# Kernel optimization log

Hardware: AMD Instinct MI355X
Metric: run time of the kernel (lower is better)

The kernel has to match this reference:

```python
import jax, jax.numpy as jnp
import numpy as np
import math

B, H, W = 4, 224, 224
NFEAT = 2048
N_SP, N_FAM, N_ORD = 200, 38, 13
THRESH = 0.5


def _conv(x, w, b, s):
    y = jax.lax.conv_general_dilated(x, w, (s, s), 'SAME', dimension_numbers=('NCHW', 'OIHW', 'NCHW'))
    return y + b[None, :, None, None]


def _features(x, bw1, bb1, bw2, bb2, bw3, bb3, bw4, bb4):
    # stride-32 CNN backbone standing in for nn.Sequential(*model.children()[:-2]) (2048-ch output)
    x = jax.nn.relu(_conv(x, bw1, bb1, 4))
    x = jax.nn.relu(_conv(x, bw2, bb2, 2))
    x = jax.nn.relu(_conv(x, bw3, bb3, 2))
    x = jax.nn.relu(_conv(x, bw4, bb4, 2))
    return x


def _resize_ac(img, y1, y2, x1, x2, oh, ow):
    # bilinear, align_corners=True resample of img[:, y1:y2, x1:x2] -> (C, oh, ow); jit-safe (gather, no dynamic shapes)
    Hh, Ww = img.shape[1], img.shape[2]
    ys = y1 + jnp.arange(oh, dtype=jnp.float32) * (y2 - 1 - y1) / (oh - 1)
    xs = x1 + jnp.arange(ow, dtype=jnp.float32) * (x2 - 1 - x1) / (ow - 1)
    ylo = jnp.clip(jnp.floor(ys).astype(jnp.int32), 0, Hh - 1)
    yhi = jnp.clip(ylo + 1, 0, Hh - 1)
    yf = (ys - ylo)[None, :, None]
    rows = img[:, ylo, :] * (1 - yf) + img[:, yhi, :] * yf
    xlo = jnp.clip(jnp.floor(xs).astype(jnp.int32), 0, Ww - 1)
    xhi = jnp.clip(xlo + 1, 0, Ww - 1)
    xf = (xs - xlo)[None, None, :]
    return rows[:, :, xlo] * (1 - xf) + rows[:, :, xhi] * xf


def _obj_loc(score, threshold):
    # vectorized, sync-free version of the torch obj_loc interval search
    n = score.shape[0]
    minsize = int(math.ceil(n * 0.125))
    defmax = int(math.ceil(n * 0.875))
    snorm = jnp.sign(score - threshold)
    cross = jnp.abs(snorm[1:] - snorm[:-1]) == 2  # crossing between j and j+1 -> index j+1 starts... torch puts index j in next interval
    ind = jnp.concatenate([cross, jnp.zeros((1,), bool)]).astype(jnp.int32)
    seg = jnp.cumsum(ind)  # segment id per position; matches torch half-open intervals [p_i, p_{i+1})
    k = jnp.sum(ind)       # number of crossings
    idx = jnp.arange(n, dtype=jnp.int32)
    seg_max = jax.ops.segment_max(score, seg, num_segments=n)
    seg_len = jax.ops.segment_sum(jnp.ones((n,), jnp.int32), seg, num_segments=n)
    seg_start = jax.ops.segment_min(idx, seg, num_segments=n)
    seg_end = jax.ops.segment_max(idx, seg, num_segments=n) + 1
    valid = (idx <= k) & (seg_len > 0)
    # torch processing order: first interval, then last, then interiors; ties keep earlier-processed
    order = jnp.where(idx == 0, 0, jnp.where(idx == k, 1, idx + 1))
    m = jnp.where(valid, seg_max, -jnp.inf)
    c1 = valid & (m == jnp.max(m))
    best_len = jnp.max(jnp.where(c1, seg_len, -1))
    c2 = c1 & (seg_len == best_len)
    sel = jnp.argmin(jnp.where(c2, order, n + 2))
    zmin, zmax = seg_start[sel], seg_end[sel]
    # min-size padding, exactly mirroring the sequential torch ifs
    pad = minsize - (zmax - zmin)
    hp = (pad + 1) // 2  # ceil(pad/2)
    need = (zmax - zmin) <= minsize
    cA = need & (zmin > hp) & (n - zmax > pad)
    zmin = jnp.where(cA, zmin - hp + 1, zmin)
    zmax = jnp.where(cA, zmax + hp, zmax)
    cB = need & (zmin < hp)
    zmin = jnp.where(cB, 0, zmin)
    zmax = jnp.where(cB, minsize, zmax)
    cC = need & (n - zmax < hp)
    zmin = jnp.where(cC, n - minsize + 1, zmin)
    zmax = jnp.where(cC, n, zmax)
    # no crossings -> fixed central window (torch early return)
    zmin = jnp.where(k == 0, minsize, zmin)
    zmax = jnp.where(k == 0, defmax, zmax)
    return zmin, zmax


def _norm01(v):
    mn, mx = v.min(), v.max()
    den = jnp.where(mx == mn, mx, mx - mn)
    num = jnp.where(mx == mn, v, v - mn)
    return num / den


def _w_h(gs, wscore, hscore, inputs, threshold):
    def one(g, wsc, hsc, img):
        top = jnp.argmax(g)  # == sort(descending)[0]
        x1, x2 = _obj_loc(_norm01(wsc[top]), threshold)
        y1, y2 = _obj_loc(_norm01(hsc[top]), threshold)
        return _resize_ac(img, y1, y2, x1, x2, img.shape[1], img.shape[2])
    return jax.vmap(one)(gs, wscore, hscore, inputs)


def _stage(gvec, fmap, inputs, wc, bc, wc1, bc1, lf_prev, bb):
    gf = gvec @ wc.T + bc  # conv1x1 on pooled feature == linear
    cam = jax.nn.sigmoid(jnp.einsum('bchw,oc->bohw', jax.lax.stop_gradient(fmap), wc) + bc[None, :, None, None])
    fh, fw = fmap.shape[2], fmap.shape[3]
    cam_up = jax.vmap(lambda im: _resize_ac(im, 0, fh, 0, fw, H, W))(cam)  # (B,C,H,W)
    wsc = cam_up.max(axis=2)  # max_pool2d((h,1)) -> (B,C,W)
    hsc = cam_up.max(axis=3)  # max_pool2d((1,w)) -> (B,C,H)
    lin = _w_h(gf, wsc, hsc, inputs, THRESH)
    la = _features(jax.lax.stop_gradient(lin), *bb)
    lf = la.mean(axis=(2, 3))  # AdaptiveAvgPool2d(1)
    ls = lf @ wc1.T + bc1
    if lf_prev is not None:
        ls = ls + (lf_prev @ wc1.T + bc1)  # bias added twice, as in torch
    return (gf + ls) / 2.0, lf


def _forward(inputs, bw1, bb1, bw2, bb2, bw3, bb3, bw4, bb4, w_ord, b_ord, w_ord1, b_ord1, w_fam, b_fam, w_fam1, b_fam1, w_sp, b_sp, w_sp1, b_sp1):
    bb = (bw1, bb1, bw2, bb2, bw3, bb3, bw4, bb4)
    fmap = _features(inputs, *bb)
    gvec = fmap.mean(axis=(2, 3))
    f_ord, lf_ord = _stage(gvec, fmap, inputs, w_ord, b_ord, w_ord1, b_ord1, None, bb)
    f_fam, lf_fam = _stage(gvec, fmap, inputs, w_fam, b_fam, w_fam1, b_fam1, lf_ord, bb)
    f_sp, _ = _stage(gvec, fmap, inputs, w_sp, b_sp, w_sp1, b_sp1, lf_fam, bb)
    return f_sp, f_fam, f_ord


def setup_inputs() -> dict:
    ks = jax.random.split(jax.random.key(0), 16)
    def he(k, shape, fan_in):
        return jax.random.normal(k, shape, jnp.float32) * np.float32(np.sqrt(2.0 / fan_in))
    d = {"inputs": jax.random.normal(ks[0], (B, 3, H, W), jnp.float32)}
    d["bw1"], d["bb1"] = he(ks[1], (256, 3, 7, 7), 3 * 49), jnp.zeros((256,), jnp.float32)
    d["bw2"], d["bb2"] = he(ks[2], (512, 256, 3, 3), 256 * 9), jnp.zeros((512,), jnp.float32)
    d["bw3"], d["bb3"] = he(ks[3], (1024, 512, 1, 1), 512), jnp.zeros((1024,), jnp.float32)
    d["bw4"], d["bb4"] = he(ks[4], (2048, 1024, 1, 1), 1024), jnp.zeros((2048,), jnp.float32)
    for i, (nm, nc) in enumerate([("ord", N_ORD), ("fam", N_FAM), ("sp", N_SP)]):
        d["w_" + nm] = he(ks[5 + 2 * i], (nc, NFEAT), NFEAT)
        d["b_" + nm] = jnp.zeros((nc,), jnp.float32)
        d["w_" + nm + "1"] = he(ks[6 + 2 * i], (nc, NFEAT), NFEAT)
        d["b_" + nm + "1"] = jnp.zeros((nc,), jnp.float32)
    return d


def reference(inputs, bw1, bb1, bw2, bb2, bw3, bb3, bw4, bb4, w_ord, b_ord, w_ord1, b_ord1, w_fam, b_fam, w_fam1, b_fam1, w_sp, b_sp, w_sp1, b_sp1):
    return _forward(inputs, bw1, bb1, bw2, bb2, bw3, bb3, bw4, bb4, w_ord, b_ord, w_ord1, b_ord1, w_fam, b_fam, w_fam1, b_fam1, w_sp, b_sp, w_sp1, b_sp1)
```

## Files before the change

### kernel.cpp

```cpp
#include <hip/hip_runtime.h>
#include <hip/hip_bf16.h>
#include <math.h>

#define TPB 256

typedef __attribute__((ext_vector_type(8))) short s16x8;
typedef __attribute__((ext_vector_type(8))) unsigned short u16x8;
typedef __attribute__((ext_vector_type(4))) float f32x4;

__global__ void conv3x3s2_k(const float* __restrict__ in, const float* __restrict__ w,
                            const float* __restrict__ bias, float* __restrict__ out, int N)
{
  int bid = blockIdx.x;
  if (N == 4) {
    const int xcd = bid & 7;
    const int n_img = xcd >> 1;
    const int kk = ((bid >> 3) << 1) | (xcd & 1);
    bid = n_img * 392 + kk;
  }
  int idx = bid * blockDim.x + threadIdx.x;
  int total = N * 512 * 28 * 7;
  if (idx >= total) return;
  int oxg = idx % 7; int t = idx / 7; int oy = t % 28; t /= 28; int oc = t % 512; int n = t / 512;
  const float* inp = in + (size_t)n * 256 * 3136;
  const float* wp = w + (size_t)oc * 2304;
  float b0 = bias[oc];
  float acc0 = b0, acc1 = b0, acc2 = b0, acc3 = b0;
  int xb0 = oxg * 8;
  #pragma unroll 4
  for (int ic = 0; ic < 256; ic++) {
    const float* ich = inp + (size_t)ic * 3136;
    const float* wr = wp + ic * 9;
    #pragma unroll
    for (int ky = 0; ky < 3; ky++) {
      int iy = oy * 2 + ky;
      if (iy >= 56) continue;
      const float* row = ich + iy * 56;
      float w0 = wr[ky * 3 + 0], w1 = wr[ky * 3 + 1], w2 = wr[ky * 3 + 2];
      {
        int xb = xb0 + 0;
        acc0 += row[xb] * w0 + row[xb + 1] * w1 + row[xb + 2] * w2;
      }
      {
        int xb = xb0 + 2;
        acc1 += row[xb] * w0 + row[xb + 1] * w1 + row[xb + 2] * w2;
      }
      {
        int xb = xb0 + 4;
        acc2 += row[xb] * w0 + row[xb + 1] * w1 + row[xb + 2] * w2;
      }
      {
        int xb = xb0 + 6;
        acc3 += row[xb] * w0 + row[xb + 1] * w1;
        if (xb + 2 < 56) acc3 += row[xb + 2] * w2;
      }
    }
  }
  float* op = out + (((size_t)n * 512 + oc) * 28 + oy) * 28 + oxg * 4;
  op[0] = fmaxf(acc0, 0.f);
  op[1] = fmaxf(acc1, 0.f);
  op[2] = fmaxf(acc2, 0.f);
  op[3] = fmaxf(acc3, 0.f);
}

template<int KH, int KW, int STRIDE, int PADL, bool BINIT>
__global__ __launch_bounds__(256)
void conv_igemm_k(const float* __restrict__ in, const float* __restrict__ w,
                  const float* __restrict__ bias, float* __restrict__ out,
                  int Cin, int Cout, int Hin, int OH, int Np, int K)
{
  __shared__ float As[16][136];
  __shared__ float Bs[16][64];

  const int tid = threadIdx.x;
  const int bx = blockIdx.x;
  const int by = blockIdx.y;
  const int OHW = OH * OH;
  const int HinHin = Hin * Hin;

  const int n_sub = tid & 63;
  const int kq = tid >> 6;
  const int n_g = bx * 64 + n_sub;
  const bool nvalid = (n_g < Np);
  const int n_c = nvalid ? n_g : 0;
  const int img = n_c / OHW;
  const int p = n_c - img * OHW;
  const int oy = p / OH;
  const int ox = p - oy * OH;
  const int iy0 = oy * STRIDE - PADL;
  const int ix0 = ox * STRIDE - PADL;
  const float* inb = in + (size_t)img * Cin * HinHin;

  const int ks = tid & 15;
  const int msq = tid >> 4;
  const int m_base = by * 128;

  const int m0 = (tid >> 4) * 8;
  const int n0 = (tid & 15) * 4;

  float acc[8][4];
  #pragma unroll
  for (int i = 0; i < 8; i++) {
    const float init = BINIT ? bias[m_base + m0 + i] : 0.f;
    #pragma unroll
    for (int j = 0; j < 4; j++) acc[i][j] = init;
  }

  const int KT = (K + 15) >> 4;
  for (int kt = 0; kt < KT; kt++) {
    const int k0 = kt * 16;
    #pragma unroll
    for (int j = 0; j < 8; j++) {
      const int m = msq + 16 * j;
      const int k = k0 + ks;
      float v = 0.f;
      if (k < K) v = w[(size_t)(m_base + m) * K + k];
      As[ks][m] = v;
    }
    #pragma unroll
    for (int j = 0; j < 4; j++) {
      const int k = k0 + kq * 4 + j;
      float v = 0.f;
      if (nvalid && k < K) {
        const int c = k / (KH * KW);
        const int r = k - c * (KH * KW);
        const int ky = r / KW;
        const int kx = r - ky * KW;
        const int iy = iy0 + ky;
        const int ix = ix0 + kx;
        if (iy >= 0 && iy < Hin && ix >= 0 && ix < Hin)
          v = inb[(size_t)c * HinHin + iy * Hin + ix];
      }
      Bs[kq * 4 + j][n_sub] = v;
    }
    __syncthreads();
    #pragma unroll
    for (int k = 0; k < 16; k++) {
      float a_[8], b_[4];
      #pragma unroll
      for (int i = 0; i < 8; i++) a_[i] = As[k][m0 + i];
      #pragma unroll
      for (int j = 0; j < 4; j++) b_[j] = Bs[k][n0 + j];
      #pragma unroll
      for (int i = 0; i < 8; i++)
        #pragma unroll
        for (int j = 0; j < 4; j++) acc[i][j] += a_[i] * b_[j];
    }
    __syncthreads();
  }

  #pragma unroll
  for (int i = 0; i < 8; i++) {
    const int m = m_base + m0 + i;
    const float bv = BINIT ? 0.f : bias[m];
    #pragma unroll
    for (int j = 0; j < 4; j++) {
      const int nn = bx * 64 + n0 + j;
      if (nn < Np) {
        const int img2 = nn / OHW;
        const int pp = nn - img2 * OHW;
        const float v = BINIT ? acc[i][j] : (acc[i][j] + bv);
        out[((size_t)img2 * Cout + m) * OHW + pp] = fmaxf(v, 0.f);
      }
    }
  }
}

__global__ void cvt_bf16_k(const float* __restrict__ in, unsigned short* __restrict__ out, int n)
{
  int i = blockIdx.x * blockDim.x + threadIdx.x;
  if (i >= n) return;
  __hip_bfloat16 h = __float2bfloat16(in[i]);
  out[i] = *reinterpret_cast<unsigned short*>(&h);
}

__global__ void cvt_bf16_pad_k(const float* __restrict__ in, unsigned short* __restrict__ out,
                               int rows, int kin, int kout)
{
  int i = blockIdx.x * blockDim.x + threadIdx.x;
  if (i >= rows * kout) return;
  int r = i / kout, k = i - r * kout;
  unsigned short v = 0;
  if (k < kin) {
    __hip_bfloat16 h = __float2bfloat16(in[(size_t)r * kin + k]);
    v = *reinterpret_cast<unsigned short*>(&h);
  }
  out[i] = v;
}

template<int KH, int KW, int STRIDE, int PADL>
__global__ __launch_bounds__(256)
void conv_mfma_k(const float* __restrict__ in, const unsigned short* __restrict__ wbf,
                 const float* __restrict__ bias, float* __restrict__ out,
                 int Cin, int Cout, int Hin, int OH, int Np, int K, int kreal)
{
  __shared__ unsigned short As[64 * 40];
  __shared__ unsigned short Bs[64 * 40];

  const int tid = threadIdx.x;
  const int bx = blockIdx.x;
  const int by = blockIdx.y;
  const int OHW = OH * OH;
  const int HH = Hin * Hin;
  const int m_base = by * 64;

  const int n_sub = tid & 63;
  const int kq = tid >> 6;
  const int n_g = bx * 64 + n_sub;
  const bool nv = (n_g < Np);
  const int n_c = nv ? n_g : 0;
  const int img = n_c / OHW;
  const int p = n_c - img * OHW;
  const int oy = p / OH;
  const int ox = p - oy * OH;
  const int iy0 = oy * STRIDE - PADL;
  const int ix0 = ox * STRIDE - PADL;
  const float* inb = in + (size_t)img * Cin * HH;

  const int arow = tid >> 2;
  const int akoff = (tid & 3) * 8;

  const int wv = tid >> 6;
  const int ln = tid & 63;
  const int lr = ln & 15;
  const int lq = ln >> 4;

  f32x4 acc[4];
  #pragma unroll
  for (int nf = 0; nf < 4; nf++) acc[nf] = (f32x4){0.f, 0.f, 0.f, 0.f};

  for (int k0 = 0; k0 < K; k0 += 32) {
    *(u16x8*)&As[arow * 40 + akoff] =
        *(const u16x8*)(wbf + (size_t)(m_base + arow) * K + k0 + akoff);
    {
      u16x8 bv;
      #pragma unroll
      for (int i = 0; i < 8; i++) {
        const int k = k0 + kq * 8 + i;
        float v = 0.f;
        if (nv && k < kreal) {
          const int c = k / (KH * KW);
          const int r = k - c * (KH * KW);
          const int ky = r / KW;
          const int kx = r - ky * KW;
          const int iy = iy0 + ky;
          const int ix = ix0 + kx;
          if (iy >= 0 && iy < Hin && ix >= 0 && ix < Hin)
            v = inb[(size_t)c * HH + iy * Hin + ix];
        }
        __hip_bfloat16 h = __float2bfloat16(v);
        bv[i] = *reinterpret_cast<unsigned short*>(&h);
      }
      *(u16x8*)&Bs[n_sub * 40 + kq * 8] = bv;
    }
    __syncthreads();

    s16x8 a = *(const s16x8*)&As[(wv * 16 + lr) * 40 + lq * 8];
    #pragma unroll
    for (int nf = 0; nf < 4; nf++) {
      s16x8 b = *(const s16x8*)&Bs[(nf * 16 + lr) * 40 + lq * 8];
      acc[nf] = __builtin_amdgcn_mfma_f32_16x16x32_bf16(a, b, acc[nf], 0, 0, 0);
    }
    __syncthreads();
  }

  #pragma unroll
  for (int nf = 0; nf < 4; nf++) {
    const int n_gl = bx * 64 + nf * 16 + lr;
    if (n_gl < Np) {
      const int img2 = n_gl / OHW;
      const int pp = n_gl - img2 * OHW;
      #pragma unroll
      for (int r = 0; r < 4; r++) {
        const int m = m_base + wv * 16 + lq * 4 + r;
        out[((size_t)img2 * Cout + m) * OHW + pp] = fmaxf(acc[nf][r] + bias[m], 0.f);
      }
    }
  }
}

__global__ void pool_k(const float* __restrict__ in, float* __restrict__ out, int total)
{
  int idx = blockIdx.x * blockDim.x + threadIdx.x;
  if (idx >= total) return;
  const float* p = in + (size_t)idx * 49;
  float s = 0.f;
  #pragma unroll
  for (int i = 0; i < 49; i++) s += p[i];
  out[idx] = s / 49.f;
}

__global__ void gf_k(const float* __restrict__ gvec,
                     const float* __restrict__ w_ord, const float* __restrict__ b_ord,
                     const float* __restrict__ w_fam, const float* __restrict__ b_fam,
                     const float* __restrict__ w_sp,  const float* __restrict__ b_sp,
                     float* __restrict__ gfbuf)
{
  int idx = blockIdx.x * blockDim.x + threadIdx.x;
  if (idx >= 12 * 256) return;
  int o = idx % 256; int t = idx / 256; int b = t % 4; int s = t / 4;
  int nc = (s == 0) ? 13 : ((s == 1) ? 38 : 200);
  if (o >= nc) return;
  const float* w = (s == 0) ? w_ord : ((s == 1) ? w_fam : w_sp);
  const float* bb = (s == 0) ? b_ord : ((s == 1) ? b_fam : b_sp);
  float acc = bb[o];
  const float* g = gvec + (size_t)b * 2048;
  const float* wr = w + (size_t)o * 2048;
  for (int c = 0; c < 2048; c++) acc += g[c] * wr[c];
  gfbuf[idx] = acc;
}

__device__ void obj_loc_dev(const float* sc, int* zmin_o, int* zmax_o)
{
  const int n = 224, minsize = 28, defmax = 196;
  float mn = sc[0], mx = sc[0];
  for (int i = 1; i < n; i++) { mn = fminf(mn, sc[i]); mx = fmaxf(mx, sc[i]); }
  float den = (mx == mn) ? mx : (mx - mn);
#define NV(i) (((mx == mn) ? sc[i] : (sc[i] - mn)) / den)
#define SGN(v) (((v) > 0.5f) ? 1 : (((v) < 0.5f) ? -1 : 0))

  int k = 0; float M = -INFINITY;
  {
    float v = NV(0); int sg = SGN(v);
    float smax = -INFINITY; int cnt = 0;
    for (int j = 0; j < n; j++) {
      int indj = 0; float vn = 0.f; int sgn_nx = 0;
      if (j < n - 1) { vn = NV(j + 1); sgn_nx = SGN(vn); int d = sgn_nx - sg; indj = (d == 2 || d == -2); }
      if (indj) { if (cnt > 0) M = fmaxf(M, smax); k++; smax = -INFINITY; cnt = 0; }
      smax = fmaxf(smax, v); cnt++;
      if (j < n - 1) { v = vn; sg = sgn_nx; }
    }
    if (cnt > 0) M = fmaxf(M, smax);
  }

  int zmin, zmax;
  if (k == 0) { zmin = minsize; zmax = defmax; }
  else {
    int bestlen = -1;
    {
      float v = NV(0); int sg = SGN(v);
      float smax = -INFINITY; int cnt = 0;
      for (int j = 0; j < n; j++) {
        int indj = 0; float vn = 0.f; int sgn_nx = 0;
        if (j < n - 1) { vn = NV(j + 1); sgn_nx = SGN(vn); int d = sgn_nx - sg; indj = (d == 2 || d == -2); }
        if (indj) { if (cnt > 0 && smax == M && cnt > bestlen) bestlen = cnt; smax = -INFINITY; cnt = 0; }
        smax = fmaxf(smax, v); cnt++;
        if (j < n - 1) { v = vn; sg = sgn_nx; }
      }
      if (cnt > 0 && smax == M && cnt > bestlen) bestlen = cnt;
    }
    int bestorder = 1 << 30; int bzmin = 0, bzmax = 0;
    {
      float v = NV(0); int sg = SGN(v);
      float smax = -INFINITY; int cnt = 0; int start = 0; int sid = 0;
      for (int j = 0; j < n; j++) {
        int indj = 0; float vn = 0.f; int sgn_nx = 0;
        if (j < n - 1) { vn = NV(j + 1); sgn_nx = SGN(vn); int d = sgn_nx - sg; indj = (d == 2 || d == -2); }
        if (indj) {
          if (cnt > 0 && smax == M && cnt == bestlen) {
            int order = (sid == 0) ? 0 : ((sid == k) ? 1 : (sid + 1));
            if (order < bestorder) { bestorder = order; bzmin = start; bzmax = j; }
          }
          sid++; start = j; smax = -INFINITY; cnt = 0;
        }
        smax = fmaxf(smax, v); cnt++;
        if (j < n - 1) { v = vn; sg = sgn_nx; }
      }
      if (cnt > 0 && smax == M && cnt == bestlen) {
        int order = (sid == 0) ? 0 : ((sid == k) ? 1 : (sid + 1));
        if (order < bestorder) { bestorder = order; bzmin = start; bzmax = n; }
      }
    }
    zmin = bzmin; zmax = bzmax;
    int pad = minsize - (zmax - zmin);
    int hp = (pad + 1) / 2;
    int need = ((zmax - zmin) <= minsize);
    if (need && (zmin > hp) && ((n - zmax) > pad)) { zmin = zmin - hp + 1; zmax = zmax + hp; }
    if (need && (zmin < hp)) { zmin = 0; zmax = minsize; }
    if (need && ((n - zmax) < hp)) { zmin = n - minsize + 1; zmax = n; }
  }
  *zmin_o = zmin; *zmax_o = zmax;
#undef NV
#undef SGN
}

__global__ void cam_k(const float* __restrict__ fmap,
                      const float* __restrict__ gfbuf,
                      const float* __restrict__ w_ord, const float* __restrict__ b_ord,
                      const float* __restrict__ w_fam, const float* __restrict__ b_fam,
                      const float* __restrict__ w_sp,  const float* __restrict__ b_sp,
                      int* __restrict__ crops)
{
  int bid = blockIdx.x;
  int s = bid / 4, b = bid % 4;
  int nc = (s == 0) ? 13 : ((s == 1) ? 38 : 200);
  const float* wc = (s == 0) ? w_ord : ((s == 1) ? w_fam : w_sp);
  const float* bc = (s == 0) ? b_ord : ((s == 1) ? b_fam : b_sp);

  __shared__ float cam7[49];
  __shared__ float wsc[224];
  __shared__ float hsc[224];
  __shared__ int top_s;
  int tid = threadIdx.x;

  if (tid == 0) {
    const float* g = gfbuf + (size_t)bid * 256;
    int best = 0; float bv = g[0];
    for (int i = 1; i < nc; i++) { if (g[i] > bv) { bv = g[i]; best = i; } }
    top_s = best;
  }
  __syncthreads();
  int top = top_s;

  if (tid < 49) {
    const float* fp = fmap + (size_t)b * 2048 * 49 + tid;
    const float* wr = wc + (size_t)top * 2048;
    float acc = bc[top];
    for (int c = 0; c < 2048; c++) acc += fp[(size_t)c * 49] * wr[c];
    cam7[tid] = 1.f / (1.f + expf(-acc));
  }
  __syncthreads();

  if (tid < 224) {
    {
      int xx = tid;
      float xsf = (float)(xx * 6) / 223.f;
      int xlo = (int)floorf(xsf); if (xlo > 6) xlo = 6; if (xlo < 0) xlo = 0;
      int xhi = xlo + 1; if (xhi > 6) xhi = 6;
      float xf = xsf - (float)xlo;
      float m = -INFINITY;
      for (int yy = 0; yy < 224; yy++) {
        float ysf = (float)(yy * 6) / 223.f;
        int ylo = (int)floorf(ysf); if (ylo > 6) ylo = 6; if (ylo < 0) ylo = 0;
        int yhi = ylo + 1; if (yhi > 6) yhi = 6;
        float yf = ysf - (float)ylo;
        float r0 = cam7[ylo * 7 + xlo] * (1.f - yf) + cam7[yhi * 7 + xlo] * yf;
        float r1 = cam7[ylo * 7 + xhi] * (1.f - yf) + cam7[yhi * 7 + xhi] * yf;
        m = fmaxf(m, r0 * (1.f - xf) + r1 * xf);
      }
      wsc[xx] = m;
    }
    {
      int yy = tid;
      float ysf = (float)(yy * 6) / 223.f;
      int ylo = (int)floorf(ysf); if (ylo > 6) ylo = 6; if (ylo < 0) ylo = 0;
      int yhi = ylo + 1; if (yhi > 6) yhi = 6;
      float yf = ysf - (float)ylo;
      float m = -INFINITY;
      for (int xx = 0; xx < 224; xx++) {
        float xsf = (float)(xx * 6) / 223.f;
        int xlo = (int)floorf(xsf); if (xlo > 6) xlo = 6; if (xlo < 0) xlo = 0;
        int xhi = xlo + 1; if (xhi > 6) xhi = 6;
        float xf = xsf - (float)xlo;
        float r0 = cam7[ylo * 7 + xlo] * (1.f - yf) + cam7[yhi * 7 + xlo] * yf;
        float r1 = cam7[ylo * 7 + xhi] * (1.f - yf) + cam7[yhi * 7 + xhi] * yf;
        m = fmaxf(m, r0 * (1.f - xf) + r1 * xf);
      }
      hsc[yy] = m;
    }
  }
  __syncthreads();

  if (tid == 0) {
    int zmin, zmax; obj_loc_dev(wsc, &zmin, &zmax);
    crops[bid * 4 + 0] = zmin; crops[bid * 4 + 1] = zmax;
  } else if (tid == 1) {
    int zmin, zmax; obj_loc_dev(hsc, &zmin, &zmax);
    crops[bid * 4 + 2] = zmin; crops[bid * 4 + 3] = zmax;
  }
}

__global__ void crop_resize_k(const float* __restrict__ in, const int* __restrict__ crops,
                              float* __restrict__ lin)
{
  int idx = blockIdx.x * blockDim.x + threadIdx.x;
  int total = 12 * 3 * 224 * 224;
  if (idx >= total) return;
  int xx = idx % 224; int t = idx / 224; int yy = t % 224; t /= 224; int c = t % 3; int img = t / 3;
  int b = img % 4;
  int x1 = crops[img * 4 + 0], x2 = crops[img * 4 + 1];
  int y1 = crops[img * 4 + 2], y2 = crops[img * 4 + 3];
  float ys = (float)y1 + (float)(yy * (y2 - 1 - y1)) / 223.f;
  float xs = (float)x1 + (float)(xx * (x2 - 1 - x1)) / 223.f;
  int ylo = (int)floorf(ys); if (ylo < 0) ylo = 0; if (ylo > 223) ylo = 223;
  int yhi = ylo + 1; if (yhi > 223) yhi = 223;
  float yf = ys - (float)ylo;
  int xlo = (int)floorf(xs); if (xlo < 0) xlo = 0; if (xlo > 223) xlo = 223;
  int xhi = xlo + 1; if (xhi > 223) xhi = 223;
  float xf = xs - (float)xlo;
  const float* im = in + ((size_t)b * 3 + c) * 50176;
  float r0 = im[ylo * 224 + xlo] * (1.f - yf) + im[yhi * 224 + xlo] * yf;
  float r1 = im[ylo * 224 + xhi] * (1.f - yf) + im[yhi * 224 + xhi] * yf;
  lin[idx] = r0 * (1.f - xf) + r1 * xf;
}

__global__ void final_k(const float* __restrict__ lf12,
                        const float* __restrict__ gfbuf,
                        const float* __restrict__ w_ord1, const float* __restrict__ b_ord1,
                        const float* __restrict__ w_fam1, const float* __restrict__ b_fam1,
                        const float* __restrict__ w_sp1,  const float* __restrict__ b_sp1,
                        float* __restrict__ out)
{
  int idx = blockIdx.x * blockDim.x + threadIdx.x;
  if (idx >= 1004) return;
  int s, b, o; const float *w1, *b1;
  if (idx < 800)      { s = 2; o = idx % 200;        b = idx / 200;        w1 = w_sp1;  b1 = b_sp1; }
  else if (idx < 952) { s = 1; o = (idx-800) % 38;   b = (idx-800) / 38;   w1 = w_fam1; b1 = b_fam1; }
  else                { s = 0; o = (idx-952) % 13;   b = (idx-952) / 13;   w1 = w_ord1; b1 = b_ord1; }
  const float* wr = w1 + (size_t)o * 2048;
  const float* lfc = lf12 + (size_t)(s * 4 + b) * 2048;
  float ls = b1[o];
  for (int c = 0; c < 2048; c++) ls += lfc[c] * wr[c];
  if (s > 0) {
    const float* lfp = lf12 + (size_t)((s - 1) * 4 + b) * 2048;
    float ls2 = b1[o];
    for (int c = 0; c < 2048; c++) ls2 += lfp[c] * wr[c];
    ls += ls2;
  }
  float gf = gfbuf[(size_t)(s * 4 + b) * 256 + o];
  out[idx] = (gf + ls) * 0.5f;
}


static inline int nblk(long long total) { return (int)((total + TPB - 1) / TPB); }
static inline int ntile(int total, int t) { return (total + t - 1) / t; }

extern "C" void kernel_launch(void* const* d_in, const int* in_sizes, int n_in,
                              void* d_out, int out_size, void* d_ws, size_t ws_size,
                              hipStream_t stream)
{
  const float* inputs = (const float*)d_in[0];
  const float* bw1 = (const float*)d_in[1];  const float* bb1 = (const float*)d_in[2];
  const float* bw2 = (const float*)d_in[3];  const float* bb2 = (const float*)d_in[4];
  const float* bw3 = (const float*)d_in[5];  const float* bb3 = (const float*)d_in[6];
  const float* bw4 = (const float*)d_in[7];  const float* bb4 = (const float*)d_in[8];
  const float* w_ord  = (const float*)d_in[9];   const float* b_ord  = (const float*)d_in[10];
  const float* w_ord1 = (const float*)d_in[11];  const float* b_ord1 = (const float*)d_in[12];
  const float* w_fam  = (const float*)d_in[13];  const float* b_fam  = (const float*)d_in[14];
  const float* w_fam1 = (const float*)d_in[15];  const float* b_fam1 = (const float*)d_in[16];
  const float* w_sp   = (const float*)d_in[17];  const float* b_sp   = (const float*)d_in[18];
  const float* w_sp1  = (const float*)d_in[19];  const float* b_sp1  = (const float*)d_in[20];
  float* out = (float*)d_out;

  float* ws = (float*)d_ws;
  size_t o_x1 = 0;
  size_t o_x2 = o_x1 + (size_t)12 * 256 * 3136;
  size_t o_x3 = o_x2 + (size_t)12 * 512 * 784;
  size_t o_x4 = o_x3 + (size_t)12 * 1024 * 196;
  size_t o_gvec = o_x4 + (size_t)12 * 2048 * 49;
  size_t o_gf = o_gvec + 4 * 2048;
  size_t o_lf = o_gf + 12 * 256;
  size_t o_crop = o_lf + 12 * 2048;
  size_t o_wbf1 = o_crop + 64;
  float* x1 = ws + o_x1;
  float* x2 = ws + o_x2;
  float* x3 = ws + o_x3;
  float* x4 = ws + o_x4;
  float* gvec = ws + o_gvec;
  float* gfbuf = ws + o_gf;
  float* lf12 = ws + o_lf;
  int* crops = (int*)(ws + o_crop);
  float* lin = ws + o_x2;
  unsigned short* wbf1 = (unsigned short*)(ws + o_wbf1);
  unsigned short* wbf2 = (unsigned short*)x3;
  unsigned short* wbf3 = (unsigned short*)x4;
  unsigned short* wbf4 = (unsigned short*)x1;

  cvt_bf16_pad_k<<<nblk(256 * 160), TPB, 0, stream>>>(bw1, wbf1, 256, 147, 160);

  {
    int np1 = 4 * 56 * 56;
    conv_igemm_k<7,7,4,1,true><<<dim3(ntile(np1,64), 2), 256, 0, stream>>>(inputs, bw1, bb1, x1, 3, 256, 224, 56, np1, 147);
    conv3x3s2_k<<<nblk((long long)4 * 512 * 28 * 7), TPB, 0, stream>>>(x1, bw2, bb2, x2, 4);
    int np3 = 4 * 14 * 14;
    conv_igemm_k<1,1,2,0,true><<<dim3(ntile(np3,64), 8), 256, 0, stream>>>(x2, bw3, bb3, x3, 512, 1024, 28, 14, np3, 512);
    int np4 = 4 * 7 * 7;
    conv_igemm_k<1,1,2,0,true><<<dim3(ntile(np4,64), 16), 256, 0, stream>>>(x3, bw4, bb4, x4, 1024, 2048, 14, 7, np4, 1024);
  }
  pool_k<<<nblk(4 * 2048), TPB, 0, stream>>>(x4, gvec, 4 * 2048);

  gf_k<<<nblk(12 * 256), TPB, 0, stream>>>(gvec, w_ord, b_ord, w_fam, b_fam, w_sp, b_sp, gfbuf);
  cam_k<<<12, TPB, 0, stream>>>(x4, gfbuf, w_ord, b_ord, w_fam, b_fam, w_sp, b_sp, crops);
  crop_resize_k<<<nblk((long long)12 * 3 * 224 * 224), TPB, 0, stream>>>(inputs, crops, lin);

  {
    int np1 = 12 * 56 * 56;
    conv_mfma_k<7,7,4,1><<<dim3(588, 4), 256, 0, stream>>>(lin, wbf1, bb1, x1, 3, 256, 224, 56, np1, 160, 147);

    cvt_bf16_k<<<nblk(512 * 2304), TPB, 0, stream>>>(bw2, wbf2, 512 * 2304);
    int np2 = 12 * 28 * 28;
    conv_mfma_k<3,3,2,0><<<dim3(147, 8), 256, 0, stream>>>(x1, wbf2, bb2, x2, 256, 512, 56, 28, np2, 2304, 2304);

    cvt_bf16_k<<<nblk(1024 * 512), TPB, 0, stream>>>(bw3, wbf3, 1024 * 512);
    int np3 = 12 * 14 * 14;
    conv_mfma_k<1,1,2,0><<<dim3(ntile(np3,64), 16), 256, 0, stream>>>(x2, wbf3, bb3, x3, 512, 1024, 28, 14, np3, 512, 512);

    cvt_bf16_k<<<nblk(2048 * 1024), TPB, 0, stream>>>(bw4, wbf4, 2048 * 1024);
    int np4 = 12 * 7 * 7;
    conv_mfma_k<1,1,2,0><<<dim3(ntile(np4,64), 32), 256, 0, stream>>>(x3, wbf4, bb4, x4, 1024, 2048, 14, 7, np4, 1024, 1024);
  }
  pool_k<<<nblk(12 * 2048), TPB, 0, stream>>>(x4, lf12, 12 * 2048);

  final_k<<<nblk(1004), TPB, 0, stream>>>(lf12, gfbuf, w_ord1, b_ord1, w_fam1, b_fam1, w_sp1, b_sp1, out);
}
```

Baseline: 2.377 ms.

## Add small-tile 1x1 conv kernel, prefetch MFMA tiles, parallelize final head

Adds a new fp32 1x1 stride-2 conv kernel with 32-row output tiles, used for the first-pass conv3/conv4. Smaller tiles launch four times as many blocks, giving more parallelism on these small problems. The MFMA conv kernel now register-prefetches the next K tile while the current one is computed, overlapping global gathers with math. The final linear head changes from one thread per output doing a 2048-long serial dot to one 64-lane wavefront per output with a shuffle reduction. The trade-offs are more blocks, and higher register pressure in the MFMA kernel.

```diff
diff --git a/kernel.cpp b/kernel.cpp
--- a/kernel.cpp
+++ b/kernel.cpp
@@ -166,6 +166,68 @@
   }
 }
 
+__global__ __launch_bounds__(256)
+void conv1x1_igemm32_k(const float* __restrict__ in, const float* __restrict__ w,
+                       const float* __restrict__ bias, float* __restrict__ out,
+                       int Cin, int Cout, int Hin, int OH, int Np)
+{
+  __shared__ float As[32][33];
+  __shared__ float Bs[32][65];
+
+  const int tid = threadIdx.x;
+  const int bx = blockIdx.x;
+  const int by = blockIdx.y;
+  const int OHW = OH * OH;
+  const int HH = Hin * Hin;
+  const int m_base = by * 32;
+
+  const int am = tid >> 3;
+  const int ak0 = (tid & 7) * 4;
+  const int bk = tid >> 3;
+  const int bn0 = (tid & 7) * 8;
+  const int cn = tid & 63;
+  const int cm0 = (tid >> 6) * 8;
+  const int n_g = bx * 64 + cn;
+
+  float acc[8];
+  #pragma unroll
+  for (int i = 0; i < 8; i++) acc[i] = bias[m_base + cm0 + i];
+
+  int bpix[8]; bool bval[8];
+  #pragma unroll
+  for (int j = 0; j < 8; j++) {
+    int n = bx * 64 + bn0 + j;
+    bval[j] = (n < Np);
+    int nn = bval[j] ? n : 0;
+    int img = nn / OHW; int pp = nn - img * OHW; int oy = pp / OH; int ox = pp - oy * OH;
+    bpix[j] = img * Cin * HH + (2 * oy) * Hin + 2 * ox;
+  }
+
+  for (int k0 = 0; k0 < Cin; k0 += 32) {
+    #pragma unroll
+    for (int j = 0; j < 4; j++)
+      As[ak0 + j][am] = w[(size_t)(m_base + am) * Cin + k0 + ak0 + j];
+    #pragma unroll
+    for (int j = 0; j < 8; j++)
+      Bs[bk][bn0 + j] = bval[j] ? in[(size_t)(k0 + bk) * HH + bpix[j]] : 0.f;
+    __syncthreads();
+    #pragma unroll
+    for (int k = 0; k < 32; k++) {
+      float b = Bs[k][cn];
+      #pragma unroll
+      for (int i = 0; i < 8; i++) acc[i] += As[k][cm0 + i] * b;
+    }
+    __syncthreads();
+  }
+
+  if (n_g < Np) {
+    int img = n_g / OHW; int pp = n_g - img * OHW;
+    #pragma unroll
+    for (int i = 0; i < 8; i++)
+      out[((size_t)img * Cout + m_base + cm0 + i) * OHW + pp] = fmaxf(acc[i], 0.f);
+  }
+}
+
 __global__ void cvt_bf16_k(const float* __restrict__ in, unsigned short* __restrict__ out, int n)
 {
   int i = blockIdx.x * blockDim.x + threadIdx.x;
@@ -229,31 +291,37 @@
   #pragma unroll
   for (int nf = 0; nf < 4; nf++) acc[nf] = (f32x4){0.f, 0.f, 0.f, 0.f};
 
+#define GATHER_TILE(K0, AV, BV)                                                   \
+  {                                                                               \
+    AV = *(const u16x8*)(wbf + (size_t)(m_base + arow) * K + (K0) + akoff);       \
+    _Pragma("unroll")                                                             \
+    for (int i = 0; i < 8; i++) {                                                 \
+      const int k = (K0) + kq * 8 + i;                                            \
+      float v = 0.f;                                                              \
+      if (nv && k < kreal) {                                                      \
+        const int c = k / (KH * KW);                                              \
+        const int r = k - c * (KH * KW);                                          \
+        const int ky = r / KW;                                                    \
+        const int kx = r - ky * KW;                                               \
+        const int iy = iy0 + ky;                                                  \
+        const int ix = ix0 + kx;                                                  \
+        if (iy >= 0 && iy < Hin && ix >= 0 && ix < Hin)                           \
+          v = inb[(size_t)c * HH + iy * Hin + ix];                                \
+      }                                                                           \
+      __hip_bfloat16 h = __float2bfloat16(v);                                     \
+      BV[i] = *reinterpret_cast<unsigned short*>(&h);                             \
+    }                                                                             \
+  }
+
+  u16x8 av, bv;
+  GATHER_TILE(0, av, bv);
+
   for (int k0 = 0; k0 < K; k0 += 32) {
-    *(u16x8*)&As[arow * 40 + akoff] =
-        *(const u16x8*)(wbf + (size_t)(m_base + arow) * K + k0 + akoff);
-    {
-      u16x8 bv;
-      #pragma unroll
-      for (int i = 0; i < 8; i++) {
-        const int k = k0 + kq * 8 + i;
-        float v = 0.f;
-        if (nv && k < kreal) {
-          const int c = k / (KH * KW);
-          const int r = k - c * (KH * KW);
-          const int ky = r / KW;
-          const int kx = r - ky * KW;
-          const int iy = iy0 + ky;
-          const int ix = ix0 + kx;
-          if (iy >= 0 && iy < Hin && ix >= 0 && ix < Hin)
-            v = inb[(size_t)c * HH + iy * Hin + ix];
-        }
-        __hip_bfloat16 h = __float2bfloat16(v);
-        bv[i] = *reinterpret_cast<unsigned short*>(&h);
-      }
-      *(u16x8*)&Bs[n_sub * 40 + kq * 8] = bv;
-    }
+    *(u16x8*)&As[arow * 40 + akoff] = av;
+    *(u16x8*)&Bs[n_sub * 40 + kq * 8] = bv;
     __syncthreads();
+
+    if (k0 + 32 < K) { GATHER_TILE(k0 + 32, av, bv); }
 
     s16x8 a = *(const s16x8*)&As[(wv * 16 + lr) * 40 + lq * 8];
     #pragma unroll
@@ -263,6 +331,7 @@
     }
     __syncthreads();
   }
+#undef GATHER_TILE
 
   #pragma unroll
   for (int nf = 0; nf < 4; nf++) {
@@ -494,31 +563,39 @@
   lin[idx] = r0 * (1.f - xf) + r1 * xf;
 }
 
-__global__ void final_k(const float* __restrict__ lf12,
-                        const float* __restrict__ gfbuf,
-                        const float* __restrict__ w_ord1, const float* __restrict__ b_ord1,
-                        const float* __restrict__ w_fam1, const float* __restrict__ b_fam1,
-                        const float* __restrict__ w_sp1,  const float* __restrict__ b_sp1,
-                        float* __restrict__ out)
-{
-  int idx = blockIdx.x * blockDim.x + threadIdx.x;
-  if (idx >= 1004) return;
+__global__ __launch_bounds__(64)
+void final_v2_k(const float* __restrict__ lf12,
+                const float* __restrict__ gfbuf,
+                const float* __restrict__ w_ord1, const float* __restrict__ b_ord1,
+                const float* __restrict__ w_fam1, const float* __restrict__ b_fam1,
+                const float* __restrict__ w_sp1,  const float* __restrict__ b_sp1,
+                float* __restrict__ out)
+{
+  int id = blockIdx.x;
+  if (id >= 1004) return;
   int s, b, o; const float *w1, *b1;
-  if (idx < 800)      { s = 2; o = idx % 200;        b = idx / 200;        w1 = w_sp1;  b1 = b_sp1; }
-  else if (idx < 952) { s = 1; o = (idx-800) % 38;   b = (idx-800) / 38;   w1 = w_fam1; b1 = b_fam1; }
-  else                { s = 0; o = (idx-952) % 13;   b = (idx-952) / 13;   w1 = w_ord1; b1 = b_ord1; }
+  if (id < 800)      { s = 2; o = id % 200;        b = id / 200;        w1 = w_sp1;  b1 = b_sp1; }
+  else if (id < 952) { s = 1; o = (id-800) % 38;   b = (id-800) / 38;   w1 = w_fam1; b1 = b_fam1; }
+  else               { s = 0; o = (id-952) % 13;   b = (id-952) / 13;   w1 = w_ord1; b1 = b_ord1; }
+  const int lane = threadIdx.x;
   const float* wr = w1 + (size_t)o * 2048;
   const float* lfc = lf12 + (size_t)(s * 4 + b) * 2048;
-  float ls = b1[o];
-  for (int c = 0; c < 2048; c++) ls += lfc[c] * wr[c];
+  float p1 = 0.f, p2 = 0.f;
+  for (int c = lane; c < 2048; c += 64) p1 = fmaf(lfc[c], wr[c], p1);
   if (s > 0) {
     const float* lfp = lf12 + (size_t)((s - 1) * 4 + b) * 2048;
-    float ls2 = b1[o];
-    for (int c = 0; c < 2048; c++) ls2 += lfp[c] * wr[c];
-    ls += ls2;
-  }
-  float gf = gfbuf[(size_t)(s * 4 + b) * 256 + o];
-  out[idx] = (gf + ls) * 0.5f;
+    for (int c = lane; c < 2048; c += 64) p2 = fmaf(lfp[c], wr[c], p2);
+  }
+  #pragma unroll
+  for (int off = 32; off > 0; off >>= 1) {
+    p1 += __shfl_down(p1, off);
+    p2 += __shfl_down(p2, off);
+  }
+  if (lane == 0) {
+    float ls = b1[o] + p1;
+    if (s > 0) ls += b1[o] + p2;
+    out[id] = (gfbuf[(size_t)(s * 4 + b) * 256 + o] + ls) * 0.5f;
+  }
 }
 
 
@@ -573,9 +650,9 @@
     conv_igemm_k<7,7,4,1,true><<<dim3(ntile(np1,64), 2), 256, 0, stream>>>(inputs, bw1, bb1, x1, 3, 256, 224, 56, np1, 147);
     conv3x3s2_k<<<nblk((long long)4 * 512 * 28 * 7), TPB, 0, stream>>>(x1, bw2, bb2, x2, 4);
     int np3 = 4 * 14 * 14;
-    conv_igemm_k<1,1,2,0,true><<<dim3(ntile(np3,64), 8), 256, 0, stream>>>(x2, bw3, bb3, x3, 512, 1024, 28, 14, np3, 512);
+    conv1x1_igemm32_k<<<dim3(ntile(np3,64), 32), 256, 0, stream>>>(x2, bw3, bb3, x3, 512, 1024, 28, 14, np3);
     int np4 = 4 * 7 * 7;
-    conv_igemm_k<1,1,2,0,true><<<dim3(ntile(np4,64), 16), 256, 0, stream>>>(x3, bw4, bb4, x4, 1024, 2048, 14, 7, np4, 1024);
+    conv1x1_igemm32_k<<<dim3(ntile(np4,64), 64), 256, 0, stream>>>(x3, bw4, bb4, x4, 1024, 2048, 14, 7, np4);
   }
   pool_k<<<nblk(4 * 2048), TPB, 0, stream>>>(x4, gvec, 4 * 2048);
 
@@ -601,5 +678,5 @@
   }
   pool_k<<<nblk(12 * 2048), TPB, 0, stream>>>(x4, lf12, 12 * 2048);
 
-  final_k<<<nblk(1004), TPB, 0, stream>>>(lf12, gfbuf, w_ord1, b_ord1, w_fam1, b_fam1, w_sp1, b_sp1, out);
-}
+  final_v2_k<<<1004, 64, 0, stream>>>(lf12, gfbuf, w_ord1, b_ord1, w_fam1, b_fam1, w_sp1, b_sp1, out);
+}
```

Result: faster. 2.098 ms (-11.7%).
